# Kernel optimization log

Hardware: AMD Instinct MI355X
Metric: run time of the kernel (lower is better)

## Reference

```python
import jax, jax.numpy as jnp
import numpy as np
from jax import lax

B, S, T = 4096, 4096, 2  # batch, seq_length, num_tags (CRF(2) hardcoded in ToNySegmenter)


def setup_inputs() -> dict:
    key = jax.random.key(0)
    k_em, k_st, k_en, k_tr, k_tg, k_len = jax.random.split(key, 6)
    emissions = jax.random.normal(k_em, (B, S, T), dtype=jnp.float32)
    start_transitions = jax.random.uniform(k_st, (T,), dtype=jnp.float32, minval=-1.0, maxval=1.0)
    end_transitions = jax.random.uniform(k_en, (T,), dtype=jnp.float32, minval=-1.0, maxval=1.0)
    transitions = jax.random.uniform(k_tr, (T, T), dtype=jnp.float32, minval=-1.0, maxval=1.0)
    tags = jax.random.randint(k_tg, (B, S), 0, T, dtype=jnp.int64)
    # variable-length sequences; first position always valid (CRF assumes mask[0]==1)
    lengths = jax.random.randint(k_len, (B,), S // 2, S + 1)
    mask = (jnp.arange(S)[None, :] < lengths[:, None]).astype(jnp.int32)
    return {
        'emissions': emissions,
        'start_transitions': start_transitions,
        'end_transitions': end_transitions,
        'transitions': transitions,
        'tags': tags,
        'mask': mask,
    }


def _crf_nll(emissions, start_transitions, end_transitions, transitions, tags, mask):
    # batch_first=True in the torch module -> transpose to time-major (S, B, ...)
    em = jnp.transpose(emissions, (1, 0, 2))      # (S, B, T)
    tg = tags.T                                   # (S, B)
    mk = mask.T.astype(em.dtype)                  # (S, B)
    seq_len, batch = tg.shape

    # ---- numerator: score of the gold path (fully vectorized over time) ----
    emit = jnp.take_along_axis(em, tg[..., None], axis=2)[..., 0]   # (S, B)
    score = start_transitions[tg[0]] + emit[0]                      # (B,)
    trans = transitions[tg[:-1], tg[1:]]                            # (S-1, B)
    score = score + jnp.sum((trans + emit[1:]) * mk[1:], axis=0)
    seq_ends = mk.sum(axis=0).astype(jnp.int32) - 1                 # (B,)
    last_tags = tg[seq_ends, jnp.arange(batch)]
    score = score + end_transitions[last_tags]

    # ---- denominator: forward algorithm via lax.scan over time ----
    init = start_transitions + em[0]                                # (B, T)

    def step(s, x):
        e_i, m_i = x                                                # (B,T), (B,)
        # s[b, prev] + transitions[prev, cur] + e_i[b, cur], logsumexp over prev
        ns = jax.nn.logsumexp(s[:, :, None] + transitions[None, :, :] + e_i[:, None, :], axis=1)
        s = jnp.where(m_i[:, None] > 0, ns, s)
        return s, None

    final, _ = lax.scan(step, init, (em[1:], mk[1:]))
    normalizer = jax.nn.logsumexp(final + end_transitions, axis=1)  # (B,)

    return -(score - normalizer).mean()


def reference(emissions, start_transitions, end_transitions, transitions, tags, mask):
    return _crf_nll(emissions, start_transitions, end_transitions, transitions, tags, mask)
```

## Files before the change

### kernel.cpp

```cpp
#include <hip/hip_runtime.h>

#define B_CONST 4096
#define S_CONST 4096

#define NEGBIG (-1e30f)

__device__ __forceinline__ float lse2(float a, float b) {
    float m = fmaxf(a, b);
    float d = fminf(a, b) - m;
    return m + __logf(1.0f + __expf(d));
}

struct Seg { float m00, m01, m10, m11; };

__device__ __forceinline__ Seg seg_compose(const Seg& L, const Seg& R) {
    Seg o;
    o.m00 = lse2(L.m00 + R.m00, L.m01 + R.m10);
    o.m01 = lse2(L.m00 + R.m01, L.m01 + R.m11);
    o.m10 = lse2(L.m10 + R.m00, L.m11 + R.m10);
    o.m11 = lse2(L.m10 + R.m01, L.m11 + R.m11);
    return o;
}

__device__ __forceinline__ int swz(int s) { return s ^ ((s >> 4) & 15); }

__global__ __launch_bounds__(1024) void crf_row_kernel(
    const float* __restrict__ em,
    const float* __restrict__ st,
    const float* __restrict__ en,
    const float* __restrict__ tr,
    const int*   __restrict__ tags,
    const int*   __restrict__ mask,
    float* __restrict__ out)
{
    const int b    = blockIdx.x;
    const int tid  = threadIdx.x;
    const int lane = tid & 63;

    const float* em_row = em   + (size_t)b * S_CONST * 2;
    const int*   tg_row = tags + (size_t)b * S_CONST;
    const int*   mk     = mask + (size_t)b * S_CONST;

    int v1 = mk[lane << 6];
    unsigned long long bal1 = __ballot(v1 != 0);
    int base = (__popcll(bal1) - 1) << 6;
    int v2 = mk[base + lane];
    const int L = base + __popcll(__ballot(v2 != 0));

    const float t00 = tr[0], t01 = tr[1], t10 = tr[2], t11 = tr[3];

    const int  c0     = tid * 4;
    const int  myHi   = min(c0 + 4, L);
    const bool active = (c0 < L);
    const int  lo     = (c0 == 0) ? 1 : c0;

    Seg seg; seg.m00 = 0.0f; seg.m11 = 0.0f; seg.m01 = NEGBIG; seg.m10 = NEGBIG;
    float sc = 0.0f;

    int4 tg4 = make_int4(0, 0, 0, 0);
    if (active) tg4 = *(const int4*)(tg_row + c0);

    int prev = __shfl_up(tg4.w, 1);
    if (lane == 0) prev = (c0 > 0 && active) ? tg_row[c0 - 1] : 0;

    if (active) {
        const float4* emv = (const float4*)(em_row + 2 * c0);
        float4 eA = emv[0];
        float4 eB = emv[1];

        #define STEP(T_, E0_, E1_, TG_)                                      \
            do {                                                             \
                int t_ = (T_);                                               \
                if (t_ >= 1 && t_ < myHi) {                                  \
                    float e0_ = (E0_), e1_ = (E1_);                          \
                    Seg M;                                                   \
                    M.m00 = t00 + e0_; M.m01 = t01 + e1_;                    \
                    M.m10 = t10 + e0_; M.m11 = t11 + e1_;                    \
                    if (t_ == lo) seg = M;                                   \
                    else          seg = seg_compose(seg, M);                 \
                    float trv = prev ? ((TG_) ? t11 : t10)                   \
                                     : ((TG_) ? t01 : t00);                  \
                    sc += trv + ((TG_) ? e1_ : e0_);                         \
                }                                                            \
                prev = (TG_);                                                \
            } while (0)

        STEP(c0 + 0, eA.x, eA.y, tg4.x);
        STEP(c0 + 1, eA.z, eA.w, tg4.y);
        STEP(c0 + 2, eB.x, eB.y, tg4.z);
        STEP(c0 + 3, eB.z, eB.w, tg4.w);
        #undef STEP
    }

    __shared__ float4 ssegs[1024];
    __shared__ float  sscs[1024];
    const int ph = swz(tid);
    ssegs[ph] = make_float4(seg.m00, seg.m01, seg.m10, seg.m11);
    sscs[ph]  = sc;
    __syncthreads();

    if (tid < 64) {
        const int s0 = tid << 4;
        float4 v = ssegs[swz(s0)];
        Seg P; P.m00 = v.x; P.m01 = v.y; P.m10 = v.z; P.m11 = v.w;
        float scT = sscs[swz(s0)];
        #pragma unroll
        for (int k = 1; k < 16; ++k) {
            const int p = swz(s0 + k);
            float4 r4 = ssegs[p];
            Seg R; R.m00 = r4.x; R.m01 = r4.y; R.m10 = r4.z; R.m11 = r4.w;
            P = seg_compose(P, R);
            scT += sscs[p];
        }

        #pragma unroll
        for (int s = 1; s < 64; s <<= 1) {
            Seg r;
            r.m00 = __shfl_down(P.m00, s);
            r.m01 = __shfl_down(P.m01, s);
            r.m10 = __shfl_down(P.m10, s);
            r.m11 = __shfl_down(P.m11, s);
            float rsc = __shfl_down(scT, s);
            P = seg_compose(P, r);
            scT += rsc;
        }

        if (tid == 0) {
            float e00 = em_row[0], e01 = em_row[1];
            float st0 = st[0], st1 = st[1];
            float en0 = en[0], en1 = en[1];

            float i0 = st0 + e00, i1 = st1 + e01;
            float f0 = lse2(i0 + P.m00, i1 + P.m10);
            float f1 = lse2(i0 + P.m01, i1 + P.m11);
            float norm = lse2(f0 + en0, f1 + en1);

            int tg0 = tg_row[0];
            int tgL = tg_row[L - 1];
            float score = (tg0 ? st1 : st0) + (tg0 ? e01 : e00) + scT
                        + (tgL ? en1 : en0);

            atomicAdd(out, (norm - score) * (1.0f / (float)B_CONST));
        }
    }
}

extern "C" void kernel_launch(void* const* d_in, const int* in_sizes, int n_in,
                              void* d_out, int out_size, void* d_ws, size_t ws_size,
                              hipStream_t stream) {
    const float* em   = (const float*)d_in[0];
    const float* st   = (const float*)d_in[1];
    const float* en   = (const float*)d_in[2];
    const float* tr   = (const float*)d_in[3];
    const int*   tags = (const int*)d_in[4];
    const int*   mask = (const int*)d_in[5];

    float* out = (float*)d_out;

    hipMemsetAsync(out, 0, sizeof(float) * out_size, stream);
    crf_row_kernel<<<B_CONST, 1024, 0, stream>>>(em, st, en, tr, tags, mask, out);
}
```

Baseline: 290.6 us.

## Use 256-thread blocks with 16 timesteps per thread and warp-level scan

Each block now uses 256 threads, and each thread processes 16 consecutive timesteps instead of 4. The cross-thread combine runs as a shuffle reduction inside each wavefront, followed by a 4-way combine in shared memory, which replaces the 1024-entry shared buffer and its serial 16-step pass. Wavefronts whose whole range lies past the sequence length skip their loads entirely. In exchange, each thread does a longer serial chain of segment compositions and holds more registers, and each thread's loads are wider, less coalesced per instruction.

```diff
diff --git a/kernel.cpp b/kernel.cpp
--- a/kernel.cpp
+++ b/kernel.cpp
@@ -22,9 +22,7 @@
     return o;
 }
 
-__device__ __forceinline__ int swz(int s) { return s ^ ((s >> 4) & 15); }
-
-__global__ __launch_bounds__(1024) void crf_row_kernel(
+__global__ __launch_bounds__(256) void crf_row_kernel(
     const float* __restrict__ em,
     const float* __restrict__ st,
     const float* __restrict__ en,
@@ -36,6 +34,9 @@
     const int b    = blockIdx.x;
     const int tid  = threadIdx.x;
     const int lane = tid & 63;
+    const int wid  = tid >> 6;
+    const int cb   = wid << 10;
+    const int c0   = cb + (lane << 4);
 
     const float* em_row = em   + (size_t)b * S_CONST * 2;
     const int*   tg_row = tags + (size_t)b * S_CONST;
@@ -49,24 +50,24 @@
 
     const float t00 = tr[0], t01 = tr[1], t10 = tr[2], t11 = tr[3];
 
-    const int  c0     = tid * 4;
-    const int  myHi   = min(c0 + 4, L);
-    const bool active = (c0 < L);
-    const int  lo     = (c0 == 0) ? 1 : c0;
-
     Seg seg; seg.m00 = 0.0f; seg.m11 = 0.0f; seg.m01 = NEGBIG; seg.m10 = NEGBIG;
     float sc = 0.0f;
 
-    int4 tg4 = make_int4(0, 0, 0, 0);
-    if (active) tg4 = *(const int4*)(tg_row + c0);
+    __shared__ float4 wseg[4];
+    __shared__ float  wsc[4];
 
-    int prev = __shfl_up(tg4.w, 1);
-    if (lane == 0) prev = (c0 > 0 && active) ? tg_row[c0 - 1] : 0;
+    if (cb < L) {
+        const int4* tv = (const int4*)(tg_row + c0);
+        int4 tq0 = tv[0], tq1 = tv[1], tq2 = tv[2], tq3 = tv[3];
+        const float4* ev = (const float4*)(em_row + 2 * c0);
+        float4 e0 = ev[0], e1 = ev[1], e2 = ev[2], e3 = ev[3];
+        float4 e4 = ev[4], e5 = ev[5], e6 = ev[6], e7 = ev[7];
 
-    if (active) {
-        const float4* emv = (const float4*)(em_row + 2 * c0);
-        float4 eA = emv[0];
-        float4 eB = emv[1];
+        int prev = __shfl_up(tq3.w, 1);
+        if (lane == 0) prev = (cb > 0) ? tg_row[cb - 1] : 0;
+
+        const int myHi = min(c0 + 16, L);
+        const int lo   = (c0 == 0) ? 1 : c0;
 
         #define STEP(T_, E0_, E1_, TG_)                                      \
             do {                                                             \
@@ -85,63 +86,70 @@
                 prev = (TG_);                                                \
             } while (0)
 
-        STEP(c0 + 0, eA.x, eA.y, tg4.x);
-        STEP(c0 + 1, eA.z, eA.w, tg4.y);
-        STEP(c0 + 2, eB.x, eB.y, tg4.z);
-        STEP(c0 + 3, eB.z, eB.w, tg4.w);
+        STEP(c0 +  0, e0.x, e0.y, tq0.x);
+        STEP(c0 +  1, e0.z, e0.w, tq0.y);
+        STEP(c0 +  2, e1.x, e1.y, tq0.z);
+        STEP(c0 +  3, e1.z, e1.w, tq0.w);
+        STEP(c0 +  4, e2.x, e2.y, tq1.x);
+        STEP(c0 +  5, e2.z, e2.w, tq1.y);
+        STEP(c0 +  6, e3.x, e3.y, tq1.z);
+        STEP(c0 +  7, e3.z, e3.w, tq1.w);
+        STEP(c0 +  8, e4.x, e4.y, tq2.x);
+        STEP(c0 +  9, e4.z, e4.w, tq2.y);
+        STEP(c0 + 10, e5.x, e5.y, tq2.z);
+        STEP(c0 + 11, e5.z, e5.w, tq2.w);
+        STEP(c0 + 12, e6.x, e6.y, tq3.x);
+        STEP(c0 + 13, e6.z, e6.w, tq3.y);
+        STEP(c0 + 14, e7.x, e7.y, tq3.z);
+        STEP(c0 + 15, e7.z, e7.w, tq3.w);
         #undef STEP
-    }
-
-    __shared__ float4 ssegs[1024];
-    __shared__ float  sscs[1024];
-    const int ph = swz(tid);
-    ssegs[ph] = make_float4(seg.m00, seg.m01, seg.m10, seg.m11);
-    sscs[ph]  = sc;
-    __syncthreads();
-
-    if (tid < 64) {
-        const int s0 = tid << 4;
-        float4 v = ssegs[swz(s0)];
-        Seg P; P.m00 = v.x; P.m01 = v.y; P.m10 = v.z; P.m11 = v.w;
-        float scT = sscs[swz(s0)];
-        #pragma unroll
-        for (int k = 1; k < 16; ++k) {
-            const int p = swz(s0 + k);
-            float4 r4 = ssegs[p];
-            Seg R; R.m00 = r4.x; R.m01 = r4.y; R.m10 = r4.z; R.m11 = r4.w;
-            P = seg_compose(P, R);
-            scT += sscs[p];
-        }
 
         #pragma unroll
         for (int s = 1; s < 64; s <<= 1) {
             Seg r;
-            r.m00 = __shfl_down(P.m00, s);
-            r.m01 = __shfl_down(P.m01, s);
-            r.m10 = __shfl_down(P.m10, s);
-            r.m11 = __shfl_down(P.m11, s);
-            float rsc = __shfl_down(scT, s);
-            P = seg_compose(P, r);
-            scT += rsc;
+            r.m00 = __shfl_down(seg.m00, s);
+            r.m01 = __shfl_down(seg.m01, s);
+            r.m10 = __shfl_down(seg.m10, s);
+            r.m11 = __shfl_down(seg.m11, s);
+            float rsc = __shfl_down(sc, s);
+            seg = seg_compose(seg, r);
+            sc += rsc;
+        }
+    }
+
+    if (lane == 0) {
+        wseg[wid] = make_float4(seg.m00, seg.m01, seg.m10, seg.m11);
+        wsc[wid]  = sc;
+    }
+    __syncthreads();
+
+    if (tid == 0) {
+        float4 v = wseg[0];
+        Seg P; P.m00 = v.x; P.m01 = v.y; P.m10 = v.z; P.m11 = v.w;
+        float scT = wsc[0];
+        #pragma unroll
+        for (int w = 1; w < 4; ++w) {
+            float4 rv = wseg[w];
+            Seg R; R.m00 = rv.x; R.m01 = rv.y; R.m10 = rv.z; R.m11 = rv.w;
+            P = seg_compose(P, R);
+            scT += wsc[w];
         }
 
-        if (tid == 0) {
-            float e00 = em_row[0], e01 = em_row[1];
-            float st0 = st[0], st1 = st[1];
-            float en0 = en[0], en1 = en[1];
+        float e00 = em_row[0], e01 = em_row[1];
+        float st0 = st[0], st1 = st[1];
+        float en0 = en[0], en1 = en[1];
 
-            float i0 = st0 + e00, i1 = st1 + e01;
-            float f0 = lse2(i0 + P.m00, i1 + P.m10);
-            float f1 = lse2(i0 + P.m01, i1 + P.m11);
-            float norm = lse2(f0 + en0, f1 + en1);
+        float i0 = st0 + e00, i1 = st1 + e01;
+        float f0 = lse2(i0 + P.m00, i1 + P.m10);
+        float f1 = lse2(i0 + P.m01, i1 + P.m11);
+        float norm = lse2(f0 + en0, f1 + en1);
 
-            int tg0 = tg_row[0];
-            int tgL = tg_row[L - 1];
-            float score = (tg0 ? st1 : st0) + (tg0 ? e01 : e00) + scT
-                        + (tgL ? en1 : en0);
+        int tg0 = tg_row[0];
+        int tgL = tg_row[L - 1];
+        float score = (tg0 ? st1 : st0) + (tg0 ? e01 : e00) + scT
+                    + (tgL ? en1 : en0);
 
-            atomicAdd(out, (norm - score) * (1.0f / (float)B_CONST));
-        }
+        atomicAdd(out, (norm - score) * (1.0f / (float)B_CONST));
     }
 }
 
@@ -158,5 +166,5 @@
     float* out = (float*)d_out;
 
     hipMemsetAsync(out, 0, sizeof(float) * out_size, stream);
-    crf_row_kernel<<<B_CONST, 1024, 0, stream>>>(em, st, en, tr, tags, mask, out);
+    crf_row_kernel<<<B_CONST, 256, 0, stream>>>(em, st, en, tr, tags, mask, out);
 }
```

After: 286.1 us. Within noise of the previous version (-1.5%).
